# Performance work log

Hardware: AMD Instinct MI355X
Metric: run time of the kernel (lower is better)

The kernel has to match this reference:

```python
import jax, jax.numpy as jnp
import numpy as np

H = 1024      # hidden_dim
NH = 16       # num_heads
HD = H // NH  # head_dim
EPS = 1e-12
SCALE = float(np.sqrt(H))


def setup_inputs() -> dict:
    key = jax.random.key(0)
    ks = jax.random.split(key, 12)
    S, B = 2048, 2
    inp = {
        "query": jax.random.normal(ks[0], (S, B, 2 * H), jnp.float32),
        "key":   jax.random.normal(ks[1], (S, B, H), jnp.float32),
        "value": jax.random.normal(ks[2], (S, B, H), jnp.float32),
        # gating params (zeros in torch init, but randomize for a meaningful test)
        "qs": jax.random.normal(ks[3], (1, 1, H), jnp.float32) * 0.02,
        "ks_p": jax.random.normal(ks[4], (1, 1, H), jnp.float32) * 0.02,
        "vs": jax.random.normal(ks[5], (1, 1, H), jnp.float32) * 0.02,
        # Overparam vq: Linear(H, 2H)
        "vq_w": jax.random.normal(ks[6], (2 * H, H), jnp.float32) * (1.0 / np.sqrt(H)),
        "vq_b": jax.random.normal(ks[7], (2 * H,), jnp.float32) * 0.02,
        # q_linear: Linear(2H, H)
        "ql_w": jax.random.normal(ks[8], (H, 2 * H), jnp.float32) * (1.0 / np.sqrt(2 * H)),
        "ql_b": jax.random.normal(ks[9], (H,), jnp.float32) * 0.02,
        # LayerNorm(H)
        "ln_g": jnp.ones((H,), jnp.float32),
        "ln_b": jnp.zeros((H,), jnp.float32),
    }
    return inp


def _layernorm(x, g, b):
    mu = jnp.mean(x, axis=-1, keepdims=True)
    var = jnp.mean(jnp.square(x - mu), axis=-1, keepdims=True)
    return (x - mu) * jax.lax.rsqrt(var + EPS) * g + b


def reference(query, key, value, qs, ks_p, vs, vq_w, vq_b, ql_w, ql_b, ln_g, ln_b):
    # gate vectors
    qsig = jax.nn.sigmoid(qs)            # [1,1,H]
    ksig = jax.nn.sigmoid(ks_p)          # [1,1,H]
    # vq = Overparam(sigmoid(vs)): c,f = l1(x).split(H); sigmoid(f)*tanh(c)
    h = jax.nn.sigmoid(vs) @ vq_w.T + vq_b   # [1,1,2H]
    c, f = h[..., :H], h[..., H:]
    vsig = jax.nn.sigmoid(f) * jnp.tanh(c)   # [1,1,H]

    q = qsig * _layernorm(query @ ql_w.T + ql_b, ln_g, ln_b)  # [S,B,H]
    k = ksig * key
    v = vsig * value

    # batch-first
    q = jnp.transpose(q, (1, 0, 2))  # [B,Q,H]
    k = jnp.transpose(k, (1, 0, 2))  # [B,K,H]
    v = jnp.transpose(v, (1, 0, 2))
    B, Q, _ = q.shape
    K = k.shape[1]

    qh = q.reshape(B, Q, NH, HD)
    kh = k.reshape(B, K, NH, HD)
    vh = v.reshape(B, K, NH, HD)

    scores = jnp.einsum('bqhd,bkhd->bhqk', qh, kh) / SCALE
    w = jax.nn.softmax(scores, axis=-1)                # [B,NH,Q,K]
    out = jnp.einsum('bhqk,bkhd->bqhd', w, vh).reshape(B, Q, H)
    # torch code's final .transpose(0,1) is not assigned -> output is [Q,B,H]
    return jnp.transpose(out, (1, 0, 2))
```

## Files before the change

kernel.cpp:

```cpp
#include <hip/hip_runtime.h>

typedef __bf16 bf16x8 __attribute__((ext_vector_type(8)));
typedef float f32x4 __attribute__((ext_vector_type(4)));
typedef unsigned short u16x8 __attribute__((ext_vector_type(8)));
typedef unsigned short u16x4 __attribute__((ext_vector_type(4)));
typedef unsigned short u16;
typedef unsigned int u32;


#define LOG2E 1.4426950408889634f

__device__ __forceinline__ float b2f(u16 u) {
  union { unsigned int i; float f; } x; x.i = ((unsigned int)u) << 16; return x.f;
}
__device__ __forceinline__ u16 f2b(float f) {
  union { float f; unsigned int i; } x; x.f = f;
  unsigned int r = (x.i + 0x7fffu + ((x.i >> 16) & 1u)) >> 16;
  return (u16)r;
}
__device__ __forceinline__ float sigm(float x) { return 1.0f / (1.0f + __expf(-x)); }
__device__ __forceinline__ u32 cvtpk(float lo, float hi) {
  u32 r; asm("v_cvt_pk_bf16_f32 %0, %1, %2" : "=v"(r) : "v"(lo), "v"(hi)); return r;
}

__device__ __forceinline__ void async16(u16* lds, const u16* g) {
  __builtin_amdgcn_global_load_lds((const __attribute__((address_space(1))) void*)g,
                                   (__attribute__((address_space(3))) void*)lds, 16, 0, 0);
}

__global__ __launch_bounds__(256) void k_cvt_all(const float4* __restrict__ q, u16x4* __restrict__ qd,
                                                 const float4* __restrict__ w, u16x4* __restrict__ wd,
                                                 const float4* __restrict__ k, u16x4* __restrict__ kd,
                                                 const float4* __restrict__ v, u16x4* __restrict__ vd) {
  int b = blockIdx.x;
  const float4* s; u16x4* d; int i;
  if (b < 8192)       { s = q; d = qd; i = b * 256 + threadIdx.x; }
  else if (b < 10240) { s = w; d = wd; i = (b - 8192) * 256 + threadIdx.x; }
  else if (b < 14336) { s = k; d = kd; i = (b - 10240) * 256 + threadIdx.x; }
  else                { s = v; d = vd; i = (b - 14336) * 256 + threadIdx.x; }
  float4 x = s[i];
  u16x4 o; o[0] = f2b(x.x); o[1] = f2b(x.y); o[2] = f2b(x.z); o[3] = f2b(x.w);
  d[i] = o;
}

__global__ __launch_bounds__(256) void k_h(const float* __restrict__ vs,
                                           const float* __restrict__ vq_w,
                                           const float* __restrict__ vq_b,
                                           float* __restrict__ h) {
  __shared__ float svs[1024];
  int t = threadIdx.x;
  for (int i = t; i < 1024; i += 256) svs[i] = sigm(vs[i]);
  __syncthreads();
  int wave = t >> 6, lane = t & 63;
  int row = blockIdx.x * 4 + wave;
  const float4* w4 = (const float4*)(vq_w + (size_t)row * 1024);
  const float4* s4 = (const float4*)svs;
  float acc = 0.f;
#pragma unroll
  for (int k = 0; k < 4; ++k) {
    float4 w = w4[k * 64 + lane];
    float4 s = s4[k * 64 + lane];
    acc += w.x * s.x + w.y * s.y + w.z * s.z + w.w * s.w;
  }
#pragma unroll
  for (int off = 1; off < 64; off <<= 1) acc += __shfl_xor(acc, off);
  if (lane == 0) h[row] = acc + vq_b[row];
}

__global__ __launch_bounds__(256) void k_gemm(const u16* __restrict__ A,
                                              const u16* __restrict__ Bt,
                                              u16* __restrict__ C) {
  __shared__ __align__(16) u16 As[128 * 32];
  __shared__ __align__(16) u16 Bs[128 * 32];
  int tid = threadIdx.x;
  int wave = tid >> 6, lane = tid & 63;
  int l15 = lane & 15, quad = lane >> 4;
  int bx = blockIdx.x & 255;
  int kh = blockIdx.x >> 8;
  int kofs = kh << 10;
  int m0 = (bx >> 3) * 128;
  int n0 = (bx & 7) * 128;
  int wm = (wave >> 1) * 64, wn = (wave & 1) * 64;
  f32x4 acc[4][4] = {};
  int c1 = tid, c2 = tid + 256;
  const u16* ga1 = A + (size_t)(m0 + (c1 >> 2)) * 2048 + kofs + (c1 & 3) * 8;
  const u16* ga2 = A + (size_t)(m0 + (c2 >> 2)) * 2048 + kofs + (c2 & 3) * 8;
  const u16* gb1 = Bt + (size_t)(n0 + (c1 >> 2)) * 2048 + kofs + (c1 & 3) * 8;
  const u16* gb2 = Bt + (size_t)(n0 + (c2 >> 2)) * 2048 + kofs + (c2 & 3) * 8;
  u16* lA1 = As + wave * 512;
  u16* lA2 = As + 2048 + wave * 512;
  u16* lB1 = Bs + wave * 512;
  u16* lB2 = Bs + 2048 + wave * 512;
  for (int kt = 0; kt < 32; ++kt) {
    async16(lA1, ga1); async16(lA2, ga2);
    async16(lB1, gb1); async16(lB2, gb2);
    ga1 += 32; ga2 += 32; gb1 += 32; gb2 += 32;
    __syncthreads();
    bf16x8 af[4], bfr[4];
#pragma unroll
    for (int mt = 0; mt < 4; ++mt)
      af[mt] = *(const bf16x8*)(As + (wm + mt * 16 + l15) * 32 + quad * 8);
#pragma unroll
    for (int nt = 0; nt < 4; ++nt)
      bfr[nt] = *(const bf16x8*)(Bs + (wn + nt * 16 + l15) * 32 + quad * 8);
#pragma unroll
    for (int mt = 0; mt < 4; ++mt)
#pragma unroll
      for (int nt = 0; nt < 4; ++nt)
        acc[mt][nt] = __builtin_amdgcn_mfma_f32_16x16x32_bf16(af[mt], bfr[nt], acc[mt][nt], 0, 0, 0);
    __syncthreads();
  }
  u16* Cp = C + (size_t)kh * 4096 * 1024;
#pragma unroll
  for (int mt = 0; mt < 4; ++mt) {
#pragma unroll
    for (int r = 0; r < 4; ++r) {
      int m = m0 + wm + mt * 16 + quad * 4 + r;
      u16* crow = Cp + (size_t)m * 1024 + n0 + wn + l15;
#pragma unroll
      for (int nt = 0; nt < 4; ++nt) crow[nt * 16] = f2b(acc[mt][nt][r]);
    }
  }
}

__global__ __launch_bounds__(256) void k_ln(const u16* __restrict__ qpre0,
                                            const u16* __restrict__ qpre1,
                                            const float* __restrict__ ql_b,
                                            const float* __restrict__ ln_g,
                                            const float* __restrict__ ln_b,
                                            const float* __restrict__ qs,
                                            const float* __restrict__ ks,
                                            u16* __restrict__ qatt) {
  int row = blockIdx.x;
  int t = threadIdx.x;
  u16x4 a4 = *(const u16x4*)(qpre0 + (size_t)row * 1024 + t * 4);
  u16x4 b4 = *(const u16x4*)(qpre1 + (size_t)row * 1024 + t * 4);
  float v[4];
  float s = 0.f, ss = 0.f;
#pragma unroll
  for (int j = 0; j < 4; ++j) {
    v[j] = b2f(a4[j]) + b2f(b4[j]) + ql_b[t * 4 + j];
    s += v[j]; ss += v[j] * v[j];
  }
#pragma unroll
  for (int off = 1; off < 64; off <<= 1) { s += __shfl_xor(s, off); ss += __shfl_xor(ss, off); }
  __shared__ float red[8];
  int wv = t >> 6, ln = t & 63;
  if (ln == 0) { red[wv] = s; red[4 + wv] = ss; }
  __syncthreads();
  s = red[0] + red[1] + red[2] + red[3];
  ss = red[4] + red[5] + red[6] + red[7];
  float mu = s * (1.f / 1024.f);
  float rstd = rsqrtf(ss * (1.f / 1024.f) - mu * mu + 1e-12f);
  int sidx = row >> 1, b = row & 1;
  int ch0 = t * 4;
  int hh = ch0 >> 6, hd0 = ch0 & 63;
  u16* dst = qatt + ((size_t)(b * 16 + hh) * 2048 + sidx) * 64 + hd0;
#pragma unroll
  for (int j = 0; j < 4; ++j) {
    int ch = ch0 + j;
    float gate = sigm(qs[ch]) * sigm(ks[ch]) * (LOG2E / 32.0f);
    float y = (v[j] - mu) * rstd * ln_g[ch] + ln_b[ch];
    dst[j] = f2b(y * gate);
  }
}

__device__ __forceinline__ f32x4 mfma16(bf16x8 a, bf16x8 b, f32x4 c) {
  return __builtin_amdgcn_mfma_f32_16x16x32_bf16(a, b, c, 0, 0, 0);
}

template <int CUR>
__device__ __forceinline__ void attn_iter(bool pref,
                                          const bf16x8 (&qf)[2][2],
                                          const u16*& kp, const u16*& vp,
                                          u16 (&Ks)[2][64 * 64], u16 (&Vt)[2][64 * 64],
                                          f32x4 (&oacc)[2][4], float (&l_i)[2],
                                          int kdst, int chbase, int pcol,
                                          int l15, int colA, int colB) {
  f32x4 sacc[2][4] = {};
  const u16* kt0 = Ks[CUR];
#pragma unroll
  for (int nt = 0; nt < 4; ++nt) {
    const u16* krow = kt0 + (nt * 16 + l15) * 64;
    bf16x8 kA = *(const bf16x8*)(krow + colA);
    bf16x8 kB = *(const bf16x8*)(krow + colB);
    sacc[0][nt] = mfma16(kA, qf[0][0], sacc[0][nt]);
    sacc[0][nt] = mfma16(kB, qf[0][1], sacc[0][nt]);
    sacc[1][nt] = mfma16(kA, qf[1][0], sacc[1][nt]);
    sacc[1][nt] = mfma16(kB, qf[1][1], sacc[1][nt]);
  }
  u16x8 kr0, kr1, va, vq;
  if (pref) {
    kp += 64 * 2048;
    kr0 = *(const u16x8*)kp;
    kr1 = *(const u16x8*)(kp + (size_t)32 * 2048);
    vp += 64 * 2048;
    va = *(const u16x8*)vp;
    vq = *(const u16x8*)(vp + 2048);
  }
  u32 pw[2][8];
#pragma unroll
  for (int f = 0; f < 2; ++f) {
    float pe[4][4];
    float ls = 0.f;
#pragma unroll
    for (int nt = 0; nt < 4; ++nt) {
#pragma unroll
      for (int r = 0; r < 4; ++r) pe[nt][r] = __builtin_amdgcn_exp2f(sacc[f][nt][r]);
      ls += (pe[nt][0] + pe[nt][1]) + (pe[nt][2] + pe[nt][3]);
    }
    l_i[f] += ls;
    pw[f][0] = cvtpk(pe[0][0], pe[0][1]); pw[f][1] = cvtpk(pe[0][2], pe[0][3]);
    pw[f][2] = cvtpk(pe[1][0], pe[1][1]); pw[f][3] = cvtpk(pe[1][2], pe[1][3]);
    pw[f][4] = cvtpk(pe[2][0], pe[2][1]); pw[f][5] = cvtpk(pe[2][2], pe[2][3]);
    pw[f][6] = cvtpk(pe[3][0], pe[3][1]); pw[f][7] = cvtpk(pe[3][2], pe[3][3]);
  }
  union U8 { u32 w[4]; bf16x8 v; };
  bf16x8 pa[2][2];
#pragma unroll
  for (int f = 0; f < 2; ++f) {
    U8 t0; t0.w[0] = pw[f][0]; t0.w[1] = pw[f][1]; t0.w[2] = pw[f][2]; t0.w[3] = pw[f][3];
    U8 t1; t1.w[0] = pw[f][4]; t1.w[1] = pw[f][5]; t1.w[2] = pw[f][6]; t1.w[3] = pw[f][7];
    pa[f][0] = t0.v; pa[f][1] = t1.v;
  }
  const u16* vt0 = Vt[CUR];
#pragma unroll
  for (int nt = 0; nt < 4; ++nt) {
    const u16* vrow = vt0 + (nt * 16 + l15) * 64;
    bf16x8 vA = *(const bf16x8*)(vrow + colA);
    bf16x8 vB = *(const bf16x8*)(vrow + colB);
    oacc[0][nt] = mfma16(pa[0][0], vA, oacc[0][nt]);
    oacc[0][nt] = mfma16(pa[0][1], vB, oacc[0][nt]);
    oacc[1][nt] = mfma16(pa[1][0], vA, oacc[1][nt]);
    oacc[1][nt] = mfma16(pa[1][1], vB, oacc[1][nt]);
  }
  if (pref) {
    u16* kd = (u16*)Ks[CUR ^ 1];
    *(u16x8*)(kd + kdst) = kr0;
    *(u16x8*)(kd + kdst + 2048) = kr1;
    u16* vd = (u16*)Vt[CUR ^ 1];
#pragma unroll
    for (int c = 0; c < 8; ++c) {
      u32 pk2 = (u32)va[c] | ((u32)vq[c] << 16);
      *(u32*)&vd[(chbase + c) * 64 + (pcol ^ (c << 3))] = pk2;
    }
  }
  __syncthreads();
}

__global__ __launch_bounds__(256, 2) void k_attn(const u16* __restrict__ qatt,
                                                 const u16* __restrict__ key,
                                                 const u16* __restrict__ value,
                                                 const float* __restrict__ hbuf,
                                                 float* __restrict__ out) {
  int bh = blockIdx.x & 31;
  int qt = blockIdx.x >> 5;
  int b = bh >> 4, h = bh & 15;
  int tid = threadIdx.x, wave = tid >> 6, lane = tid & 63;
  int l15 = lane & 15, quad = lane >> 4;
  int q0 = qt * 128;

  __shared__ __align__(16) u16 Ks[2][64 * 64];
  __shared__ __align__(16) u16 Vt[2][64 * 64];

  bf16x8 qf[2][2];
#pragma unroll
  for (int f = 0; f < 2; ++f) {
    const u16* qrow = qatt + ((size_t)bh * 2048 + q0 + f * 64 + wave * 16 + l15) * 64 + quad * 8;
    qf[f][0] = *(const bf16x8*)qrow;
    qf[f][1] = *(const bf16x8*)(qrow + 32);
  }

  const u16* kb = key + (size_t)b * 1024 + (size_t)h * 64;
  const u16* vb = value + (size_t)b * 1024 + (size_t)h * 64;

  int krow = tid >> 3;
  int kchk = (tid & 7) * 8;
  const u16* kp = kb + (size_t)krow * 2048 + kchk;
  int kdst = krow * 64 + (kchk ^ ((krow & 7) << 3));

  int p = lane & 31;
  int chbase = wave * 16 + (lane >> 5) * 8;
  const u16* vp = vb + (size_t)2 * p * 2048 + chbase;
  int kk = 2 * p;
  int pcol = ((kk >> 5) & 1) * 32 + ((kk >> 2) & 3) * 8 + ((kk >> 4) & 1) * 4 + (kk & 3);
  int swr = (l15 & 7) << 3;
  int colA = (8 * quad) ^ swr;
  int colB = (32 + 8 * quad) ^ swr;

  {
    u16x8 kr0 = *(const u16x8*)kp;
    u16x8 kr1 = *(const u16x8*)(kp + (size_t)32 * 2048);
    *(u16x8*)(&Ks[0][kdst]) = kr0;
    *(u16x8*)(&Ks[0][kdst + 2048]) = kr1;
    u16x8 va = *(const u16x8*)vp;
    u16x8 vq = *(const u16x8*)(vp + 2048);
#pragma unroll
    for (int c = 0; c < 8; ++c) {
      u32 pk2 = (u32)va[c] | ((u32)vq[c] << 16);
      *(u32*)&Vt[0][(chbase + c) * 64 + (pcol ^ (c << 3))] = pk2;
    }
  }
  __syncthreads();

  f32x4 oacc[2][4] = {};
  float l_i[2] = {};

  for (int kt = 0; kt < 32; kt += 2) {
    attn_iter<0>(true, qf, kp, vp, Ks, Vt, oacc, l_i, kdst, chbase, pcol, l15, colA, colB);
    attn_iter<1>(kt < 30, qf, kp, vp, Ks, Vt, oacc, l_i, kdst, chbase, pcol, l15, colA, colB);
  }

#pragma unroll
  for (int f = 0; f < 2; ++f) {
    float l = l_i[f];
    l += __shfl_xor(l, 16);
    l += __shfl_xor(l, 32);
    l_i[f] = l;
  }
  float vsg[4];
#pragma unroll
  for (int nt = 0; nt < 4; ++nt) {
    int ch = h * 64 + nt * 16 + l15;
    vsg[nt] = sigm(hbuf[1024 + ch]) * tanhf(hbuf[ch]);
  }
#pragma unroll
  for (int f = 0; f < 2; ++f)
#pragma unroll
    for (int r = 0; r < 4; ++r) {
      int sq = q0 + f * 64 + wave * 16 + quad * 4 + r;
      float inv = 1.0f / __shfl(l_i[f], quad * 4 + r);
      float* orow = out + ((size_t)sq * 2 + b) * 1024 + h * 64;
#pragma unroll
      for (int nt = 0; nt < 4; ++nt)
        orow[nt * 16 + l15] = oacc[f][nt][r] * inv * vsg[nt];
    }
}

extern "C" void kernel_launch(void* const* d_in, const int* in_sizes, int n_in,
                              void* d_out, int out_size, void* d_ws, size_t ws_size,
                              hipStream_t stream) {
  (void)in_sizes; (void)n_in; (void)out_size; (void)ws_size;
  const float* query = (const float*)d_in[0];
  const float* key   = (const float*)d_in[1];
  const float* value = (const float*)d_in[2];
  const float* qs    = (const float*)d_in[3];
  const float* ksp   = (const float*)d_in[4];
  const float* vs    = (const float*)d_in[5];
  const float* vq_w  = (const float*)d_in[6];
  const float* vq_b  = (const float*)d_in[7];
  const float* ql_w  = (const float*)d_in[8];
  const float* ql_b  = (const float*)d_in[9];
  const float* ln_g  = (const float*)d_in[10];
  const float* ln_b  = (const float*)d_in[11];
  float* out = (float*)d_out;

  float* ws = (float*)d_ws;
  float* h   = ws;
  u16* qpre  = (u16*)(ws + 4096);
  u16* qbf   = qpre + (size_t)2 * 4096 * 1024;
  u16* qatt  = qbf;
  u16* wbf   = qbf + (size_t)4096 * 2048;
  u16* kbf   = wbf + (size_t)1024 * 2048;
  u16* vbf   = kbf + (size_t)4096 * 1024;

  hipLaunchKernelGGL(k_cvt_all, dim3(18432), dim3(256), 0, stream,
                     (const float4*)query, (u16x4*)qbf,
                     (const float4*)ql_w,  (u16x4*)wbf,
                     (const float4*)key,   (u16x4*)kbf,
                     (const float4*)value, (u16x4*)vbf);
  hipLaunchKernelGGL(k_h,    dim3(512),  dim3(256), 0, stream, vs, vq_w, vq_b, h);
  hipLaunchKernelGGL(k_gemm, dim3(512),  dim3(256), 0, stream, qbf, wbf, qpre);
  hipLaunchKernelGGL(k_ln,   dim3(4096), dim3(256), 0, stream, qpre, qpre + (size_t)4096 * 1024,
                     ql_b, ln_g, ln_b, qs, ksp, qatt);
  hipLaunchKernelGGL(k_attn, dim3(512),  dim3(256), 0, stream, qatt, kbf, vbf, h, out);
}
```

Before: 222.0 us.

## Fuse prep kernels, shrink GEMM tile, vectorize LayerNorm, add MFMA priority hints

Merges the fp32-to-bf16 conversion, the vq gate GEMV and a precomputed q/k gate vector into one grid-stride launch, removing a kernel launch. The split-K GEMM tile drops from 128x128 to 64x128 so twice as many blocks run. LayerNorm now gives each wave one row with 16-wide vector loads and stores, so the shared-memory reduction and sync go away, and it reads the precomputed gate instead of recomputing sigmoids. The attention loop wraps its MFMA sections in s_setprio. Smaller GEMM tiles lower data reuse per block, and the fused prep kernel mixes unequal work across blocks.

```diff
diff --git a/kernel.cpp b/kernel.cpp
--- a/kernel.cpp
+++ b/kernel.cpp
@@ -28,83 +28,93 @@
                                    (__attribute__((address_space(3))) void*)lds, 16, 0, 0);
 }
 
-__global__ __launch_bounds__(256) void k_cvt_all(const float4* __restrict__ q, u16x4* __restrict__ qd,
-                                                 const float4* __restrict__ w, u16x4* __restrict__ wd,
-                                                 const float4* __restrict__ k, u16x4* __restrict__ kd,
-                                                 const float4* __restrict__ v, u16x4* __restrict__ vd) {
+__global__ __launch_bounds__(256) void k_cvt_h(const float4* __restrict__ q, u16x4* __restrict__ qd,
+                                               const float4* __restrict__ w, u16x4* __restrict__ wd,
+                                               const float4* __restrict__ k, u16x4* __restrict__ kd,
+                                               const float4* __restrict__ v, u16x4* __restrict__ vd,
+                                               const float* __restrict__ vs,
+                                               const float* __restrict__ vq_w,
+                                               const float* __restrict__ vq_b,
+                                               float* __restrict__ h,
+                                               const float* __restrict__ qs,
+                                               const float* __restrict__ ks,
+                                               float* __restrict__ gate) {
+  __shared__ float svs[1024];
   int b = blockIdx.x;
-  const float4* s; u16x4* d; int i;
-  if (b < 8192)       { s = q; d = qd; i = b * 256 + threadIdx.x; }
-  else if (b < 10240) { s = w; d = wd; i = (b - 8192) * 256 + threadIdx.x; }
-  else if (b < 14336) { s = k; d = kd; i = (b - 10240) * 256 + threadIdx.x; }
-  else                { s = v; d = vd; i = (b - 14336) * 256 + threadIdx.x; }
-  float4 x = s[i];
-  u16x4 o; o[0] = f2b(x.x); o[1] = f2b(x.y); o[2] = f2b(x.z); o[3] = f2b(x.w);
-  d[i] = o;
-}
-
-__global__ __launch_bounds__(256) void k_h(const float* __restrict__ vs,
-                                           const float* __restrict__ vq_w,
-                                           const float* __restrict__ vq_b,
-                                           float* __restrict__ h) {
-  __shared__ float svs[1024];
   int t = threadIdx.x;
-  for (int i = t; i < 1024; i += 256) svs[i] = sigm(vs[i]);
-  __syncthreads();
-  int wave = t >> 6, lane = t & 63;
-  int row = blockIdx.x * 4 + wave;
-  const float4* w4 = (const float4*)(vq_w + (size_t)row * 1024);
-  const float4* s4 = (const float4*)svs;
-  float acc = 0.f;
-#pragma unroll
-  for (int k = 0; k < 4; ++k) {
-    float4 w = w4[k * 64 + lane];
-    float4 s = s4[k * 64 + lane];
-    acc += w.x * s.x + w.y * s.y + w.z * s.z + w.w * s.w;
-  }
-#pragma unroll
-  for (int off = 1; off < 64; off <<= 1) acc += __shfl_xor(acc, off);
-  if (lane == 0) h[row] = acc + vq_b[row];
+  if (b < 2048) {
+#pragma unroll
+    for (int vb = b; vb < 18432; vb += 2048) {
+      const float4* s; u16x4* d; int i;
+      if (vb < 8192)       { s = q; d = qd; i = vb * 256 + t; }
+      else if (vb < 10240) { s = w; d = wd; i = (vb - 8192) * 256 + t; }
+      else if (vb < 14336) { s = k; d = kd; i = (vb - 10240) * 256 + t; }
+      else                 { s = v; d = vd; i = (vb - 14336) * 256 + t; }
+      float4 x = s[i];
+      u16x4 o; o[0] = f2b(x.x); o[1] = f2b(x.y); o[2] = f2b(x.z); o[3] = f2b(x.w);
+      d[i] = o;
+    }
+    return;
+  }
+  if (b < 2560) {
+    for (int i = t; i < 1024; i += 256) svs[i] = sigm(vs[i]);
+    __syncthreads();
+    int wave = t >> 6, lane = t & 63;
+    int row = (b - 2048) * 4 + wave;
+    const float4* w4 = (const float4*)(vq_w + (size_t)row * 1024);
+    const float4* s4 = (const float4*)svs;
+    float acc = 0.f;
+#pragma unroll
+    for (int kk = 0; kk < 4; ++kk) {
+      float4 wv = w4[kk * 64 + lane];
+      float4 sv = s4[kk * 64 + lane];
+      acc += wv.x * sv.x + wv.y * sv.y + wv.z * sv.z + wv.w * sv.w;
+    }
+#pragma unroll
+    for (int off = 1; off < 64; off <<= 1) acc += __shfl_xor(acc, off);
+    if (lane == 0) h[row] = acc + vq_b[row];
+    return;
+  }
+  int ch = (b - 2560) * 256 + t;
+  gate[ch] = sigm(qs[ch]) * sigm(ks[ch]) * (LOG2E / 32.0f);
 }
 
 __global__ __launch_bounds__(256) void k_gemm(const u16* __restrict__ A,
                                               const u16* __restrict__ Bt,
                                               u16* __restrict__ C) {
-  __shared__ __align__(16) u16 As[128 * 32];
+  __shared__ __align__(16) u16 As[64 * 32];
   __shared__ __align__(16) u16 Bs[128 * 32];
   int tid = threadIdx.x;
   int wave = tid >> 6, lane = tid & 63;
   int l15 = lane & 15, quad = lane >> 4;
-  int bx = blockIdx.x & 255;
-  int kh = blockIdx.x >> 8;
+  int bx = blockIdx.x & 511;
+  int kh = blockIdx.x >> 9;
   int kofs = kh << 10;
-  int m0 = (bx >> 3) * 128;
+  int m0 = (bx >> 3) * 64;
   int n0 = (bx & 7) * 128;
-  int wm = (wave >> 1) * 64, wn = (wave & 1) * 64;
-  f32x4 acc[4][4] = {};
+  int wm = (wave >> 1) * 32, wn = (wave & 1) * 64;
+  f32x4 acc[2][4] = {};
   int c1 = tid, c2 = tid + 256;
-  const u16* ga1 = A + (size_t)(m0 + (c1 >> 2)) * 2048 + kofs + (c1 & 3) * 8;
-  const u16* ga2 = A + (size_t)(m0 + (c2 >> 2)) * 2048 + kofs + (c2 & 3) * 8;
+  const u16* gaA = A + (size_t)(m0 + (c1 >> 2)) * 2048 + kofs + (c1 & 3) * 8;
   const u16* gb1 = Bt + (size_t)(n0 + (c1 >> 2)) * 2048 + kofs + (c1 & 3) * 8;
   const u16* gb2 = Bt + (size_t)(n0 + (c2 >> 2)) * 2048 + kofs + (c2 & 3) * 8;
   u16* lA1 = As + wave * 512;
-  u16* lA2 = As + 2048 + wave * 512;
   u16* lB1 = Bs + wave * 512;
   u16* lB2 = Bs + 2048 + wave * 512;
   for (int kt = 0; kt < 32; ++kt) {
-    async16(lA1, ga1); async16(lA2, ga2);
+    async16(lA1, gaA);
     async16(lB1, gb1); async16(lB2, gb2);
-    ga1 += 32; ga2 += 32; gb1 += 32; gb2 += 32;
+    gaA += 32; gb1 += 32; gb2 += 32;
     __syncthreads();
-    bf16x8 af[4], bfr[4];
-#pragma unroll
-    for (int mt = 0; mt < 4; ++mt)
+    bf16x8 af[2], bfr[4];
+#pragma unroll
+    for (int mt = 0; mt < 2; ++mt)
       af[mt] = *(const bf16x8*)(As + (wm + mt * 16 + l15) * 32 + quad * 8);
 #pragma unroll
     for (int nt = 0; nt < 4; ++nt)
       bfr[nt] = *(const bf16x8*)(Bs + (wn + nt * 16 + l15) * 32 + quad * 8);
 #pragma unroll
-    for (int mt = 0; mt < 4; ++mt)
+    for (int mt = 0; mt < 2; ++mt)
 #pragma unroll
       for (int nt = 0; nt < 4; ++nt)
         acc[mt][nt] = __builtin_amdgcn_mfma_f32_16x16x32_bf16(af[mt], bfr[nt], acc[mt][nt], 0, 0, 0);
@@ -112,7 +122,7 @@
   }
   u16* Cp = C + (size_t)kh * 4096 * 1024;
 #pragma unroll
-  for (int mt = 0; mt < 4; ++mt) {
+  for (int mt = 0; mt < 2; ++mt) {
 #pragma unroll
     for (int r = 0; r < 4; ++r) {
       int m = m0 + wm + mt * 16 + quad * 4 + r;
@@ -128,41 +138,52 @@
                                             const float* __restrict__ ql_b,
                                             const float* __restrict__ ln_g,
                                             const float* __restrict__ ln_b,
-                                            const float* __restrict__ qs,
-                                            const float* __restrict__ ks,
+                                            const float* __restrict__ gate,
                                             u16* __restrict__ qatt) {
-  int row = blockIdx.x;
   int t = threadIdx.x;
-  u16x4 a4 = *(const u16x4*)(qpre0 + (size_t)row * 1024 + t * 4);
-  u16x4 b4 = *(const u16x4*)(qpre1 + (size_t)row * 1024 + t * 4);
-  float v[4];
+  int wave = t >> 6, lane = t & 63;
+  int row = blockIdx.x * 4 + wave;
+  int ch0 = lane * 16;
+  const u16* p0 = qpre0 + (size_t)row * 1024 + ch0;
+  const u16* p1 = qpre1 + (size_t)row * 1024 + ch0;
+  u16x8 a0 = *(const u16x8*)p0;
+  u16x8 a1 = *(const u16x8*)(p0 + 8);
+  u16x8 c0 = *(const u16x8*)p1;
+  u16x8 c1 = *(const u16x8*)(p1 + 8);
+  float qb[16];
+#pragma unroll
+  for (int i = 0; i < 4; ++i) *(float4*)&qb[i * 4] = *(const float4*)(ql_b + ch0 + i * 4);
+  float v[16];
   float s = 0.f, ss = 0.f;
 #pragma unroll
-  for (int j = 0; j < 4; ++j) {
-    v[j] = b2f(a4[j]) + b2f(b4[j]) + ql_b[t * 4 + j];
-    s += v[j]; ss += v[j] * v[j];
-  }
+  for (int j = 0; j < 8; ++j) {
+    v[j] = b2f(a0[j]) + b2f(c0[j]) + qb[j];
+    v[8 + j] = b2f(a1[j]) + b2f(c1[j]) + qb[8 + j];
+  }
+#pragma unroll
+  for (int j = 0; j < 16; ++j) { s += v[j]; ss += v[j] * v[j]; }
 #pragma unroll
   for (int off = 1; off < 64; off <<= 1) { s += __shfl_xor(s, off); ss += __shfl_xor(ss, off); }
-  __shared__ float red[8];
-  int wv = t >> 6, ln = t & 63;
-  if (ln == 0) { red[wv] = s; red[4 + wv] = ss; }
-  __syncthreads();
-  s = red[0] + red[1] + red[2] + red[3];
-  ss = red[4] + red[5] + red[6] + red[7];
   float mu = s * (1.f / 1024.f);
   float rstd = rsqrtf(ss * (1.f / 1024.f) - mu * mu + 1e-12f);
+  float g_[16], bb[16], gt[16];
+#pragma unroll
+  for (int i = 0; i < 4; ++i) {
+    *(float4*)&g_[i * 4] = *(const float4*)(ln_g + ch0 + i * 4);
+    *(float4*)&bb[i * 4] = *(const float4*)(ln_b + ch0 + i * 4);
+    *(float4*)&gt[i * 4] = *(const float4*)(gate + ch0 + i * 4);
+  }
   int sidx = row >> 1, b = row & 1;
-  int ch0 = t * 4;
   int hh = ch0 >> 6, hd0 = ch0 & 63;
   u16* dst = qatt + ((size_t)(b * 16 + hh) * 2048 + sidx) * 64 + hd0;
-#pragma unroll
-  for (int j = 0; j < 4; ++j) {
-    int ch = ch0 + j;
-    float gate = sigm(qs[ch]) * sigm(ks[ch]) * (LOG2E / 32.0f);
-    float y = (v[j] - mu) * rstd * ln_g[ch] + ln_b[ch];
-    dst[j] = f2b(y * gate);
-  }
+  u16x8 o0, o1;
+#pragma unroll
+  for (int j = 0; j < 8; ++j) {
+    o0[j] = f2b(((v[j] - mu) * rstd * g_[j] + bb[j]) * gt[j]);
+    o1[j] = f2b(((v[8 + j] - mu) * rstd * g_[8 + j] + bb[8 + j]) * gt[8 + j]);
+  }
+  *(u16x8*)dst = o0;
+  *(u16x8*)(dst + 8) = o1;
 }
 
 __device__ __forceinline__ f32x4 mfma16(bf16x8 a, bf16x8 b, f32x4 c) {
@@ -179,6 +200,7 @@
                                           int l15, int colA, int colB) {
   f32x4 sacc[2][4] = {};
   const u16* kt0 = Ks[CUR];
+  __builtin_amdgcn_s_setprio(1);
 #pragma unroll
   for (int nt = 0; nt < 4; ++nt) {
     const u16* krow = kt0 + (nt * 16 + l15) * 64;
@@ -189,6 +211,7 @@
     sacc[1][nt] = mfma16(kA, qf[1][0], sacc[1][nt]);
     sacc[1][nt] = mfma16(kB, qf[1][1], sacc[1][nt]);
   }
+  __builtin_amdgcn_s_setprio(0);
   u16x8 kr0, kr1, va, vq;
   if (pref) {
     kp += 64 * 2048;
@@ -224,6 +247,7 @@
     pa[f][0] = t0.v; pa[f][1] = t1.v;
   }
   const u16* vt0 = Vt[CUR];
+  __builtin_amdgcn_s_setprio(1);
 #pragma unroll
   for (int nt = 0; nt < 4; ++nt) {
     const u16* vrow = vt0 + (nt * 16 + l15) * 64;
@@ -234,6 +258,7 @@
     oacc[1][nt] = mfma16(pa[1][0], vA, oacc[1][nt]);
     oacc[1][nt] = mfma16(pa[1][1], vB, oacc[1][nt]);
   }
+  __builtin_amdgcn_s_setprio(0);
   if (pref) {
     u16* kd = (u16*)Ks[CUR ^ 1];
     *(u16x8*)(kd + kdst) = kr0;
@@ -356,7 +381,8 @@
   float* out = (float*)d_out;
 
   float* ws = (float*)d_ws;
-  float* h   = ws;
+  float* h    = ws;
+  float* gate = ws + 2048;
   u16* qpre  = (u16*)(ws + 4096);
   u16* qbf   = qpre + (size_t)2 * 4096 * 1024;
   u16* qatt  = qbf;
@@ -364,14 +390,14 @@
   u16* kbf   = wbf + (size_t)1024 * 2048;
   u16* vbf   = kbf + (size_t)4096 * 1024;
 
-  hipLaunchKernelGGL(k_cvt_all, dim3(18432), dim3(256), 0, stream,
+  hipLaunchKernelGGL(k_cvt_h, dim3(2564), dim3(256), 0, stream,
                      (const float4*)query, (u16x4*)qbf,
                      (const float4*)ql_w,  (u16x4*)wbf,
                      (const float4*)key,   (u16x4*)kbf,
-                     (const float4*)value, (u16x4*)vbf);
-  hipLaunchKernelGGL(k_h,    dim3(512),  dim3(256), 0, stream, vs, vq_w, vq_b, h);
-  hipLaunchKernelGGL(k_gemm, dim3(512),  dim3(256), 0, stream, qbf, wbf, qpre);
-  hipLaunchKernelGGL(k_ln,   dim3(4096), dim3(256), 0, stream, qpre, qpre + (size_t)4096 * 1024,
-                     ql_b, ln_g, ln_b, qs, ksp, qatt);
+                     (const float4*)value, (u16x4*)vbf,
+                     vs, vq_w, vq_b, h, qs, ksp, gate);
+  hipLaunchKernelGGL(k_gemm, dim3(1024), dim3(256), 0, stream, qbf, wbf, qpre);
+  hipLaunchKernelGGL(k_ln,   dim3(1024), dim3(256), 0, stream, qpre, qpre + (size_t)4096 * 1024,
+                     ql_b, ln_g, ln_b, gate, qatt);
   hipLaunchKernelGGL(k_attn, dim3(512),  dim3(256), 0, stream, qatt, kbf, vbf, h, out);
 }
```

New measurement: 215.3 us. 1.03x faster.
